# Optimization experiments

Measured on AMD Instinct MI355X. Metric: run time of the kernel, lower is better.

## Reference

```python
import jax, jax.numpy as jnp
import numpy as np

N_NODES = 50000


def gcn_conv(x, src, dst, W, b, n):
    # PyG GCNConv: h = x @ W; add self-loops; sym-norm aggregate; + bias
    h = x @ W
    loop = jnp.arange(n, dtype=src.dtype)
    s = jnp.concatenate([src, loop])
    d = jnp.concatenate([dst, loop])
    deg = jax.ops.segment_sum(jnp.ones(s.shape[0], h.dtype), d, num_segments=n)
    dinv = jnp.where(deg > 0, jax.lax.rsqrt(deg), 0.0)
    norm = dinv[s] * dinv[d]  # [E+n]
    msg = h[s] * norm[:, None]  # [E+n, C] gather
    out = jax.ops.segment_sum(msg, d, num_segments=n)  # scatter-add
    return out + b


def mlp_decode(z, src, dst, Wa, ba, Wb, bb):
    feat = jnp.concatenate([z[src], z[dst]], axis=1)  # [P, 2*out]
    hid = jax.nn.relu(feat @ Wa + ba)
    return hid @ Wb + bb  # [P, 1]


def setup_inputs() -> dict:
    key = jax.random.key(0)
    ks = jax.random.split(key, 12)
    in_c, hid_c, out_c = 128, 128, 64
    E, P = 800000, 200000
    x = jax.random.normal(ks[0], (N_NODES, in_c), dtype=jnp.float32)
    edge_index = jax.random.randint(ks[1], (2, E), 0, N_NODES, dtype=jnp.int64)
    pos_edge_index = jax.random.randint(ks[2], (2, P), 0, N_NODES, dtype=jnp.int64)
    neg_edge_index = jax.random.randint(ks[3], (2, P), 0, N_NODES, dtype=jnp.int64)
    s1 = 1.0 / np.sqrt(in_c)
    s2 = 1.0 / np.sqrt(hid_c)
    s3 = 1.0 / np.sqrt(2 * out_c)
    W1 = jax.random.uniform(ks[4], (in_c, hid_c), jnp.float32, -s1, s1)
    b1 = jnp.zeros((hid_c,), jnp.float32)
    W2 = jax.random.uniform(ks[5], (hid_c, out_c), jnp.float32, -s2, s2)
    b2 = jnp.zeros((out_c,), jnp.float32)
    Wa = jax.random.uniform(ks[6], (2 * out_c, hid_c), jnp.float32, -s3, s3)
    ba = jax.random.uniform(ks[7], (hid_c,), jnp.float32, -s3, s3)
    Wb = jax.random.uniform(ks[8], (hid_c, 1), jnp.float32, -s2, s2)
    bb = jax.random.uniform(ks[9], (1,), jnp.float32, -s2, s2)
    return {"x": x, "edge_index": edge_index, "pos_edge_index": pos_edge_index,
            "neg_edge_index": neg_edge_index, "W1": W1, "b1": b1, "W2": W2,
            "b2": b2, "Wa": Wa, "ba": ba, "Wb": Wb, "bb": bb}


def reference(x, edge_index, pos_edge_index, neg_edge_index,
              W1, b1, W2, b2, Wa, ba, Wb, bb):
    src, dst = edge_index[0], edge_index[1]
    n = x.shape[0]
    z = gcn_conv(x, src, dst, W1, b1, n)
    z = jax.nn.relu(z)  # dropout disabled in eval mode
    z = gcn_conv(z, src, dst, W2, b2, n)
    pos_pred = mlp_decode(z, pos_edge_index[0], pos_edge_index[1], Wa, ba, Wb, bb)
    neg_pred = mlp_decode(z, neg_edge_index[0], neg_edge_index[1], Wa, ba, Wb, bb)
    return (pos_pred, neg_pred)
```

## Files before the change

kernel.cpp:

```cpp
#include <hip/hip_runtime.h>
#include <hip/hip_bf16.h>

#define NODES 50000
#define NEDGE 800000
#define NPRED 200000

typedef __attribute__((ext_vector_type(8))) short bf16x8;
typedef __attribute__((ext_vector_type(8))) unsigned short u16x8;
typedef __attribute__((ext_vector_type(4))) float f32x4;

__device__ inline float bf2f(unsigned short u) {
    union { unsigned int i; float f; } v; v.i = ((unsigned int)u) << 16; return v.f;
}
__device__ inline unsigned short f2bf(float f) {
    __hip_bfloat16 b = __float2bfloat16(f);
    return *(unsigned short*)&b;
}

__global__ __launch_bounds__(256) void deg_init(int* __restrict__ deg, int* __restrict__ fillc, int n) {
    int i = blockIdx.x * 256 + threadIdx.x;
    if (i < n) { deg[i] = 1; fillc[i] = 0; }
}

__global__ __launch_bounds__(256) void deg_count(const int* __restrict__ dstv, int* __restrict__ deg, int E) {
    int e = blockIdx.x * 256 + threadIdx.x;
    if (e < E) atomicAdd(&deg[dstv[e]], 1);
}

__global__ __launch_bounds__(256) void scan_bsum(const int* __restrict__ deg, int* __restrict__ bsum, int n) {
    __shared__ int s[256];
    int t = threadIdx.x, b = blockIdx.x;
    int base = b * 1024 + t * 4;
    int sum = 0;
#pragma unroll
    for (int j = 0; j < 4; ++j) { int i = base + j; if (i < n) sum += deg[i] - 1; }
    s[t] = sum; __syncthreads();
    for (int off = 128; off >= 1; off >>= 1) {
        if (t < off) s[t] += s[t + off];
        __syncthreads();
    }
    if (t == 0) bsum[b] = s[0];
}

__global__ void scan_boff(const int* __restrict__ bsum, int* __restrict__ boff, int nb,
                          int* __restrict__ row_ptr, int n) {
    int t = threadIdx.x;
    int v = (t < nb) ? bsum[t] : 0;
    int orig = v;
    for (int off = 1; off < 64; off <<= 1) {
        int u = __shfl_up(v, off, 64);
        if (t >= off) v += u;
    }
    boff[t] = v - orig;
    if (t == 63) row_ptr[n] = v;
}

__global__ __launch_bounds__(256) void scan_write(const int* __restrict__ deg, const int* __restrict__ boff,
                                                  int* __restrict__ row_ptr, float* __restrict__ dinv, int n) {
    __shared__ int s[256];
    int t = threadIdx.x, b = blockIdx.x;
    int base = b * 1024 + t * 4;
    int v[4]; int sum = 0;
#pragma unroll
    for (int j = 0; j < 4; ++j) { int i = base + j; v[j] = (i < n) ? (deg[i] - 1) : 0; sum += v[j]; }
    s[t] = sum; __syncthreads();
    for (int off = 1; off < 256; off <<= 1) {
        int u = (t >= off) ? s[t - off] : 0;
        __syncthreads();
        s[t] += u;
        __syncthreads();
    }
    int run = s[t] - sum + boff[b];
#pragma unroll
    for (int j = 0; j < 4; ++j) {
        int i = base + j;
        if (i < n) { row_ptr[i] = run; run += v[j]; dinv[i] = rsqrtf((float)deg[i]); }
    }
}

__global__ __launch_bounds__(256) void csr_fill(const int* __restrict__ ei, const int* __restrict__ row_ptr,
                                                int* __restrict__ fillc, int* __restrict__ colv, int E) {
    int e = blockIdx.x * 256 + threadIdx.x;
    if (e < E) {
        int s = ei[e];
        int d = ei[E + e];
        int p = row_ptr[d] + atomicAdd(&fillc[d], 1);
        colv[p] = s;
    }
}

__global__ __launch_bounds__(256) void perm_all(const float* __restrict__ W1, const float* __restrict__ W2,
                                                const float* __restrict__ Wa,
                                                unsigned short* __restrict__ pW1,
                                                unsigned short* __restrict__ pW2,
                                                unsigned short* __restrict__ pWa) {
    int t = blockIdx.x * 256 + threadIdx.x;
    if (t >= 5120) return;
    const float* W; unsigned short* P; int N;
    if (t < 2048)      { W = W1; P = pW1; N = 128; }
    else if (t < 3072) { W = W2; P = pW2; N = 64;  t -= 2048; }
    else               { W = Wa; P = pWa; N = 128; t -= 3072; }
    int lane = t & 63;
    int kt = (t >> 6) & 3;
    int nt = t >> 8;
    int n = nt * 16 + (lane & 15);
    int k0 = kt * 32 + (lane >> 4) * 8;
#pragma unroll
    for (int j = 0; j < 8; ++j) P[t * 8 + j] = f2bf(W[(k0 + j) * N + n]);
}

template <int NT, bool AFP32>
__global__ __launch_bounds__(256) void gemm_mfma(const void* __restrict__ Xv,
                                                 const unsigned short* __restrict__ perm,
                                                 unsigned short* __restrict__ H, int M) {
    int w = blockIdx.x * 4 + (threadIdx.x >> 6);
    int m0 = w * 16;
    if (m0 >= M) return;
    int lane = threadIdx.x & 63;
    int m = lane & 15, q = lane >> 4;
    size_t row = (size_t)(m0 + m);
    bf16x8 a[4];
    if (AFP32) {
        const float* X = (const float*)Xv;
#pragma unroll
        for (int kt = 0; kt < 4; ++kt) {
            float4 f0 = *(const float4*)&X[row * 128 + kt * 32 + q * 8];
            float4 f1 = *(const float4*)&X[row * 128 + kt * 32 + q * 8 + 4];
            bf16x8 av;
            av[0] = (short)f2bf(f0.x); av[1] = (short)f2bf(f0.y);
            av[2] = (short)f2bf(f0.z); av[3] = (short)f2bf(f0.w);
            av[4] = (short)f2bf(f1.x); av[5] = (short)f2bf(f1.y);
            av[6] = (short)f2bf(f1.z); av[7] = (short)f2bf(f1.w);
            a[kt] = av;
        }
    } else {
        const unsigned short* X = (const unsigned short*)Xv;
#pragma unroll
        for (int kt = 0; kt < 4; ++kt)
            a[kt] = *(const bf16x8*)&X[row * 128 + kt * 32 + q * 8];
    }
    const int N = NT * 16;
#pragma unroll
    for (int nt = 0; nt < NT; ++nt) {
        f32x4 c = {0.f, 0.f, 0.f, 0.f};
#pragma unroll
        for (int kt = 0; kt < 4; ++kt) {
            bf16x8 b = *(const bf16x8*)(perm + (size_t)((nt * 4 + kt) * 64 + lane) * 8);
            c = __builtin_amdgcn_mfma_f32_16x16x32_bf16(a[kt], b, c, 0, 0, 0);
        }
#pragma unroll
        for (int r = 0; r < 4; ++r)
            H[(size_t)(m0 + q * 4 + r) * N + nt * 16 + m] = f2bf(c[r]);
    }
}

template <int C, bool RELU>
__global__ __launch_bounds__(256) void agg_bf16(const unsigned short* __restrict__ h,
                                                const int* __restrict__ row_ptr, const int* __restrict__ colv,
                                                const float* __restrict__ dinv, const float* __restrict__ bias,
                                                unsigned short* __restrict__ out) {
    constexpr int TPN = C / 8;
    constexpr int NPB = 256 / TPN;
    int d = blockIdx.x * NPB + threadIdx.x / TPN;
    if (d >= NODES) return;
    int c8 = (threadIdx.x % TPN) * 8;
    float dv = dinv[d];
    float acc[8];
    u16x8 self = *(const u16x8*)&h[(size_t)d * C + c8];
#pragma unroll
    for (int j = 0; j < 8; ++j) acc[j] = bf2f(self[j]) * dv;
    int i = row_ptr[d], end = row_ptr[d + 1];
    for (; i + 3 < end; i += 4) {
        int s0 = colv[i], s1 = colv[i + 1], s2 = colv[i + 2], s3 = colv[i + 3];
        float w0 = dinv[s0], w1 = dinv[s1], w2 = dinv[s2], w3 = dinv[s3];
        u16x8 r0 = *(const u16x8*)&h[(size_t)s0 * C + c8];
        u16x8 r1 = *(const u16x8*)&h[(size_t)s1 * C + c8];
        u16x8 r2 = *(const u16x8*)&h[(size_t)s2 * C + c8];
        u16x8 r3 = *(const u16x8*)&h[(size_t)s3 * C + c8];
#pragma unroll
        for (int j = 0; j < 8; ++j)
            acc[j] += bf2f(r0[j]) * w0 + bf2f(r1[j]) * w1 + bf2f(r2[j]) * w2 + bf2f(r3[j]) * w3;
    }
    for (; i < end; ++i) {
        int s0 = colv[i];
        float w0 = dinv[s0];
        u16x8 r0 = *(const u16x8*)&h[(size_t)s0 * C + c8];
#pragma unroll
        for (int j = 0; j < 8; ++j) acc[j] += bf2f(r0[j]) * w0;
    }
    u16x8 ov;
#pragma unroll
    for (int j = 0; j < 8; ++j) {
        float o = acc[j] * dv + bias[c8 + j];
        if (RELU) o = fmaxf(o, 0.f);
        ov[j] = f2bf(o);
    }
    *(u16x8*)&out[(size_t)d * C + c8] = ov;
}

__global__ __launch_bounds__(256) void decode_mfma(const unsigned short* __restrict__ zb,
                                                   const int* __restrict__ pos, const int* __restrict__ neg,
                                                   const unsigned short* __restrict__ perm,
                                                   const float* __restrict__ ba, const float* __restrict__ Wb,
                                                   const float* __restrict__ bb, float* __restrict__ out, int P) {
    int lane = threadIdx.x & 63;
    int w = blockIdx.x * 4 + (threadIdx.x >> 6);
    int half = (w >= 6250);
    const int* src = half ? neg : pos;
    float* o = out + (half ? P : 0);
    int e0 = (half ? (w - 6250) : w) * 32;
    int m = lane & 15, q = lane >> 4;
    int eA = e0 + m, eB = e0 + 16 + m;
    int sA = src[eA], dA = src[P + eA];
    int sB = src[eB], dB = src[P + eB];
    bf16x8 a0[4], a1[4];
    a0[0] = *(const bf16x8*)(zb + (size_t)sA * 64 + q * 8);
    a0[1] = *(const bf16x8*)(zb + (size_t)sA * 64 + 32 + q * 8);
    a0[2] = *(const bf16x8*)(zb + (size_t)dA * 64 + q * 8);
    a0[3] = *(const bf16x8*)(zb + (size_t)dA * 64 + 32 + q * 8);
    a1[0] = *(const bf16x8*)(zb + (size_t)sB * 64 + q * 8);
    a1[1] = *(const bf16x8*)(zb + (size_t)sB * 64 + 32 + q * 8);
    a1[2] = *(const bf16x8*)(zb + (size_t)dB * 64 + q * 8);
    a1[3] = *(const bf16x8*)(zb + (size_t)dB * 64 + 32 + q * 8);
    float p0[4] = {0.f, 0.f, 0.f, 0.f};
    float p1[4] = {0.f, 0.f, 0.f, 0.f};
#pragma unroll
    for (int nt = 0; nt < 8; ++nt) {
        f32x4 c0 = {0.f, 0.f, 0.f, 0.f};
        f32x4 c1 = {0.f, 0.f, 0.f, 0.f};
#pragma unroll
        for (int kt = 0; kt < 4; ++kt) {
            bf16x8 b = *(const bf16x8*)(perm + (size_t)((nt * 4 + kt) * 64 + lane) * 8);
            c0 = __builtin_amdgcn_mfma_f32_16x16x32_bf16(a0[kt], b, c0, 0, 0, 0);
            c1 = __builtin_amdgcn_mfma_f32_16x16x32_bf16(a1[kt], b, c1, 0, 0, 0);
        }
        int ch = nt * 16 + m;
        float bav = ba[ch], wbv = Wb[ch];
#pragma unroll
        for (int r = 0; r < 4; ++r) {
            p0[r] += fmaxf(c0[r] + bav, 0.f) * wbv;
            p1[r] += fmaxf(c1[r] + bav, 0.f) * wbv;
        }
    }
#pragma unroll
    for (int off = 8; off >= 1; off >>= 1) {
#pragma unroll
        for (int r = 0; r < 4; ++r) {
            p0[r] += __shfl_xor(p0[r], off, 64);
            p1[r] += __shfl_xor(p1[r], off, 64);
        }
    }
    if (m == 0) {
        float bbv = bb[0];
#pragma unroll
        for (int r = 0; r < 4; ++r) {
            o[e0 + q * 4 + r] = p0[r] + bbv;
            o[e0 + 16 + q * 4 + r] = p1[r] + bbv;
        }
    }
}

extern "C" void kernel_launch(void* const* d_in, const int* in_sizes, int n_in,
                              void* d_out, int out_size, void* d_ws, size_t ws_size,
                              hipStream_t stream) {
    const int N = NODES, E = NEDGE, P = NPRED;
    const float* x  = (const float*)d_in[0];
    const int*   ei = (const int*)d_in[1];
    const int*  pos = (const int*)d_in[2];
    const int*  neg = (const int*)d_in[3];
    const float* W1 = (const float*)d_in[4];
    const float* b1 = (const float*)d_in[5];
    const float* W2 = (const float*)d_in[6];
    const float* b2 = (const float*)d_in[7];
    const float* Wa = (const float*)d_in[8];
    const float* ba = (const float*)d_in[9];
    const float* Wb = (const float*)d_in[10];
    const float* bb = (const float*)d_in[11];
    float* out = (float*)d_out;

    char* w = (char*)d_ws;
    auto alloc = [&](size_t bytes) { char* p = w; w += (bytes + 255) & ~(size_t)255; return p; };
    int*   deg     = (int*)alloc((size_t)N * 4);
    int*   fillc   = (int*)alloc((size_t)N * 4);
    int*   row_ptr = (int*)alloc((size_t)(N + 1) * 4);
    int*   colv    = (int*)alloc((size_t)E * 4);
    float* dinv    = (float*)alloc((size_t)N * 4);
    int*   bsum    = (int*)alloc(64 * 4);
    int*   boff    = (int*)alloc(64 * 4);
    unsigned short* h1b = (unsigned short*)alloc((size_t)N * 128 * 2);
    unsigned short* z1b = (unsigned short*)alloc((size_t)N * 128 * 2);
    unsigned short* h2b = (unsigned short*)alloc((size_t)N * 64 * 2);
    unsigned short* zb  = (unsigned short*)alloc((size_t)N * 64 * 2);
    unsigned short* pW1 = (unsigned short*)alloc(2048 * 8 * 2);
    unsigned short* pW2 = (unsigned short*)alloc(1024 * 8 * 2);
    unsigned short* pWa = (unsigned short*)alloc(2048 * 8 * 2);

    const int nb = (N + 1023) / 1024;
    deg_init<<<(N + 255) / 256, 256, 0, stream>>>(deg, fillc, N);
    deg_count<<<(E + 255) / 256, 256, 0, stream>>>(ei + E, deg, E);
    scan_bsum<<<nb, 256, 0, stream>>>(deg, bsum, N);
    scan_boff<<<1, 64, 0, stream>>>(bsum, boff, nb, row_ptr, N);
    scan_write<<<nb, 256, 0, stream>>>(deg, boff, row_ptr, dinv, N);
    csr_fill<<<(E + 255) / 256, 256, 0, stream>>>(ei, row_ptr, fillc, colv, E);

    perm_all<<<20, 256, 0, stream>>>(W1, W2, Wa, pW1, pW2, pWa);

    gemm_mfma<8, true><<<782, 256, 0, stream>>>(x, pW1, h1b, N);
    agg_bf16<128, true><<<N / 16, 256, 0, stream>>>(h1b, row_ptr, colv, dinv, b1, z1b);

    gemm_mfma<4, false><<<782, 256, 0, stream>>>(z1b, pW2, h2b, N);
    agg_bf16<64, false><<<(N + 31) / 32, 256, 0, stream>>>(h2b, row_ptr, colv, dinv, b2, zb);

    decode_mfma<<<3125, 256, 0, stream>>>(zb, pos, neg, pWa, ba, Wb, bb, out, P);
}
```

Before: 285.8 us.

## Precompute per-node decoder projections and decode edges by gathering U and V

The edge MLP's first layer is split algebraically: concat(z[s],z[d])@Wa becomes z[s]@Wa_top + z[d]@Wa_bot. Both halves are computed once per node (50k rows) in fp16 instead of per edge (400k edges). Each edge then gathers two 128-wide fp16 rows and does only bias, relu and a dot with Wb. The CSR build is also simplified: the fill counters start at row_ptr, and degrees are counted with vectorized int4 loads. This removes redundant MFMA work at the cost of extra per-node memory traffic, larger per-edge gathers, and fp16 rounding of the intermediate.

After: 289.1 us. About the same (+1.2%).

```diff
diff --git a/kernel.cpp b/kernel.cpp
--- a/kernel.cpp
+++ b/kernel.cpp
@@ -1,5 +1,6 @@
 #include <hip/hip_runtime.h>
 #include <hip/hip_bf16.h>
+#include <hip/hip_fp16.h>
 
 #define NODES 50000
 #define NEDGE 800000
@@ -16,15 +17,27 @@
     __hip_bfloat16 b = __float2bfloat16(f);
     return *(unsigned short*)&b;
 }
-
-__global__ __launch_bounds__(256) void deg_init(int* __restrict__ deg, int* __restrict__ fillc, int n) {
+__device__ inline float h2f(unsigned short u) {
+    __half h = *(__half*)&u; return __half2float(h);
+}
+__device__ inline unsigned short f2h(float f) {
+    __half h = __float2half(f); return *(unsigned short*)&h;
+}
+
+__global__ __launch_bounds__(256) void deg_init(int* __restrict__ deg, int n) {
     int i = blockIdx.x * 256 + threadIdx.x;
-    if (i < n) { deg[i] = 1; fillc[i] = 0; }
-}
-
-__global__ __launch_bounds__(256) void deg_count(const int* __restrict__ dstv, int* __restrict__ deg, int E) {
-    int e = blockIdx.x * 256 + threadIdx.x;
-    if (e < E) atomicAdd(&deg[dstv[e]], 1);
+    if (i < n) deg[i] = 1;
+}
+
+__global__ __launch_bounds__(256) void deg_count4(const int* __restrict__ dstv, int* __restrict__ deg, int E4) {
+    int i = blockIdx.x * 256 + threadIdx.x;
+    if (i < E4) {
+        int4 d4 = ((const int4*)dstv)[i];
+        atomicAdd(&deg[d4.x], 1);
+        atomicAdd(&deg[d4.y], 1);
+        atomicAdd(&deg[d4.z], 1);
+        atomicAdd(&deg[d4.w], 1);
+    }
 }
 
 __global__ __launch_bounds__(256) void scan_bsum(const int* __restrict__ deg, int* __restrict__ bsum, int n) {
@@ -56,7 +69,8 @@
 }
 
 __global__ __launch_bounds__(256) void scan_write(const int* __restrict__ deg, const int* __restrict__ boff,
-                                                  int* __restrict__ row_ptr, float* __restrict__ dinv, int n) {
+                                                  int* __restrict__ row_ptr, int* __restrict__ fillc,
+                                                  float* __restrict__ dinv, int n) {
     __shared__ int s[256];
     int t = threadIdx.x, b = blockIdx.x;
     int base = b * 1024 + t * 4;
@@ -74,17 +88,20 @@
 #pragma unroll
     for (int j = 0; j < 4; ++j) {
         int i = base + j;
-        if (i < n) { row_ptr[i] = run; run += v[j]; dinv[i] = rsqrtf((float)deg[i]); }
-    }
-}
-
-__global__ __launch_bounds__(256) void csr_fill(const int* __restrict__ ei, const int* __restrict__ row_ptr,
+        if (i < n) {
+            row_ptr[i] = run; fillc[i] = run; run += v[j];
+            dinv[i] = rsqrtf((float)deg[i]);
+        }
+    }
+}
+
+__global__ __launch_bounds__(256) void csr_fill(const int* __restrict__ ei,
                                                 int* __restrict__ fillc, int* __restrict__ colv, int E) {
     int e = blockIdx.x * 256 + threadIdx.x;
     if (e < E) {
         int s = ei[e];
         int d = ei[E + e];
-        int p = row_ptr[d] + atomicAdd(&fillc[d], 1);
+        int p = atomicAdd(&fillc[d], 1);
         colv[p] = s;
     }
 }
@@ -96,17 +113,29 @@
                                                 unsigned short* __restrict__ pWa) {
     int t = blockIdx.x * 256 + threadIdx.x;
     if (t >= 5120) return;
-    const float* W; unsigned short* P; int N;
-    if (t < 2048)      { W = W1; P = pW1; N = 128; }
-    else if (t < 3072) { W = W2; P = pW2; N = 64;  t -= 2048; }
-    else               { W = Wa; P = pWa; N = 128; t -= 3072; }
-    int lane = t & 63;
-    int kt = (t >> 6) & 3;
-    int nt = t >> 8;
-    int n = nt * 16 + (lane & 15);
-    int k0 = kt * 32 + (lane >> 4) * 8;
-#pragma unroll
-    for (int j = 0; j < 8; ++j) P[t * 8 + j] = f2bf(W[(k0 + j) * N + n]);
+    if (t < 3072) {
+        const float* W; unsigned short* P; int N;
+        if (t < 2048) { W = W1; P = pW1; N = 128; }
+        else          { W = W2; P = pW2; N = 64; t -= 2048; }
+        int lane = t & 63;
+        int kt = (t >> 6) & 3;
+        int nt = t >> 8;
+        int n = nt * 16 + (lane & 15);
+        int k0 = kt * 32 + (lane >> 4) * 8;
+#pragma unroll
+        for (int j = 0; j < 8; ++j) P[t * 8 + j] = f2bf(W[(k0 + j) * N + n]);
+    } else {
+        int tt = t - 3072;
+        int h = tt >> 10;
+        int r = tt & 1023;
+        int lane = r & 63;
+        int kt = (r >> 6) & 1;
+        int nt = r >> 7;
+        int n = nt * 16 + (lane & 15);
+        int k0 = h * 64 + kt * 32 + (lane >> 4) * 8;
+#pragma unroll
+        for (int j = 0; j < 8; ++j) pWa[tt * 8 + j] = f2bf(Wa[(k0 + j) * 128 + n]);
+    }
 }
 
 template <int NT, bool AFP32>
@@ -198,66 +227,71 @@
     *(u16x8*)&out[(size_t)d * C + c8] = ov;
 }
 
-__global__ __launch_bounds__(256) void decode_mfma(const unsigned short* __restrict__ zb,
+__global__ __launch_bounds__(256) void uv_gemm(const unsigned short* __restrict__ zb,
+                                               const unsigned short* __restrict__ pWa,
+                                               unsigned short* __restrict__ U, unsigned short* __restrict__ V,
+                                               int M) {
+    int w = blockIdx.x * 4 + (threadIdx.x >> 6);
+    int m0 = w * 16;
+    if (m0 >= M) return;
+    int lane = threadIdx.x & 63;
+    int m = lane & 15, q = lane >> 4;
+    size_t row = (size_t)(m0 + m);
+    bf16x8 a0 = *(const bf16x8*)&zb[row * 64 + q * 8];
+    bf16x8 a1 = *(const bf16x8*)&zb[row * 64 + 32 + q * 8];
+#pragma unroll
+    for (int h = 0; h < 2; ++h) {
+        unsigned short* O = h ? V : U;
+        const unsigned short* p = pWa + (size_t)h * 1024 * 8;
+#pragma unroll
+        for (int nt = 0; nt < 8; ++nt) {
+            bf16x8 b0 = *(const bf16x8*)(p + (size_t)((nt * 2 + 0) * 64 + lane) * 8);
+            bf16x8 b1 = *(const bf16x8*)(p + (size_t)((nt * 2 + 1) * 64 + lane) * 8);
+            f32x4 c = {0.f, 0.f, 0.f, 0.f};
+            c = __builtin_amdgcn_mfma_f32_16x16x32_bf16(a0, b0, c, 0, 0, 0);
+            c = __builtin_amdgcn_mfma_f32_16x16x32_bf16(a1, b1, c, 0, 0, 0);
+#pragma unroll
+            for (int r = 0; r < 4; ++r)
+                O[(size_t)(m0 + q * 4 + r) * 128 + nt * 16 + m] = f2h(c[r]);
+        }
+    }
+}
+
+__global__ __launch_bounds__(256) void edge_decode(const unsigned short* __restrict__ U,
+                                                   const unsigned short* __restrict__ V,
                                                    const int* __restrict__ pos, const int* __restrict__ neg,
-                                                   const unsigned short* __restrict__ perm,
                                                    const float* __restrict__ ba, const float* __restrict__ Wb,
                                                    const float* __restrict__ bb, float* __restrict__ out, int P) {
-    int lane = threadIdx.x & 63;
-    int w = blockIdx.x * 4 + (threadIdx.x >> 6);
-    int half = (w >= 6250);
+    __shared__ float sba[128], sWb[128];
+    int tid = threadIdx.x;
+    if (tid < 128) sba[tid] = ba[tid];
+    else sWb[tid - 128] = Wb[tid - 128];
+    __syncthreads();
+    int half = (blockIdx.x >= 6250);
     const int* src = half ? neg : pos;
     float* o = out + (half ? P : 0);
-    int e0 = (half ? (w - 6250) : w) * 32;
-    int m = lane & 15, q = lane >> 4;
-    int eA = e0 + m, eB = e0 + 16 + m;
-    int sA = src[eA], dA = src[P + eA];
-    int sB = src[eB], dB = src[P + eB];
-    bf16x8 a0[4], a1[4];
-    a0[0] = *(const bf16x8*)(zb + (size_t)sA * 64 + q * 8);
-    a0[1] = *(const bf16x8*)(zb + (size_t)sA * 64 + 32 + q * 8);
-    a0[2] = *(const bf16x8*)(zb + (size_t)dA * 64 + q * 8);
-    a0[3] = *(const bf16x8*)(zb + (size_t)dA * 64 + 32 + q * 8);
-    a1[0] = *(const bf16x8*)(zb + (size_t)sB * 64 + q * 8);
-    a1[1] = *(const bf16x8*)(zb + (size_t)sB * 64 + 32 + q * 8);
-    a1[2] = *(const bf16x8*)(zb + (size_t)dB * 64 + q * 8);
-    a1[3] = *(const bf16x8*)(zb + (size_t)dB * 64 + 32 + q * 8);
-    float p0[4] = {0.f, 0.f, 0.f, 0.f};
-    float p1[4] = {0.f, 0.f, 0.f, 0.f};
-#pragma unroll
-    for (int nt = 0; nt < 8; ++nt) {
-        f32x4 c0 = {0.f, 0.f, 0.f, 0.f};
-        f32x4 c1 = {0.f, 0.f, 0.f, 0.f};
-#pragma unroll
-        for (int kt = 0; kt < 4; ++kt) {
-            bf16x8 b = *(const bf16x8*)(perm + (size_t)((nt * 4 + kt) * 64 + lane) * 8);
-            c0 = __builtin_amdgcn_mfma_f32_16x16x32_bf16(a0[kt], b, c0, 0, 0, 0);
-            c1 = __builtin_amdgcn_mfma_f32_16x16x32_bf16(a1[kt], b, c1, 0, 0, 0);
-        }
-        int ch = nt * 16 + m;
-        float bav = ba[ch], wbv = Wb[ch];
-#pragma unroll
-        for (int r = 0; r < 4; ++r) {
-            p0[r] += fmaxf(c0[r] + bav, 0.f) * wbv;
-            p1[r] += fmaxf(c1[r] + bav, 0.f) * wbv;
-        }
-    }
-#pragma unroll
-    for (int off = 8; off >= 1; off >>= 1) {
-#pragma unroll
-        for (int r = 0; r < 4; ++r) {
-            p0[r] += __shfl_xor(p0[r], off, 64);
-            p1[r] += __shfl_xor(p1[r], off, 64);
-        }
-    }
-    if (m == 0) {
-        float bbv = bb[0];
-#pragma unroll
-        for (int r = 0; r < 4; ++r) {
-            o[e0 + q * 4 + r] = p0[r] + bbv;
-            o[e0 + 16 + q * 4 + r] = p1[r] + bbv;
-        }
-    }
+    int b = half ? (int)blockIdx.x - 6250 : (int)blockIdx.x;
+    int lane = tid & 63;
+    int wv = tid >> 6;
+    int e = b * 32 + wv * 8 + (lane >> 3);
+    int ch0 = (lane & 7) * 16;
+    int s = src[e], d = src[P + e];
+    u16x8 u0 = *(const u16x8*)&U[(size_t)s * 128 + ch0];
+    u16x8 u1 = *(const u16x8*)&U[(size_t)s * 128 + ch0 + 8];
+    u16x8 v0 = *(const u16x8*)&V[(size_t)d * 128 + ch0];
+    u16x8 v1 = *(const u16x8*)&V[(size_t)d * 128 + ch0 + 8];
+    float acc = 0.f;
+#pragma unroll
+    for (int j = 0; j < 8; ++j) {
+        float a = h2f(u0[j]) + h2f(v0[j]) + sba[ch0 + j];
+        acc += fmaxf(a, 0.f) * sWb[ch0 + j];
+        float c = h2f(u1[j]) + h2f(v1[j]) + sba[ch0 + 8 + j];
+        acc += fmaxf(c, 0.f) * sWb[ch0 + 8 + j];
+    }
+    acc += __shfl_xor(acc, 1, 64);
+    acc += __shfl_xor(acc, 2, 64);
+    acc += __shfl_xor(acc, 4, 64);
+    if ((lane & 7) == 0) o[e] = acc + bb[0];
 }
 
 extern "C" void kernel_launch(void* const* d_in, const int* in_sizes, int n_in,
@@ -291,17 +325,19 @@
     unsigned short* z1b = (unsigned short*)alloc((size_t)N * 128 * 2);
     unsigned short* h2b = (unsigned short*)alloc((size_t)N * 64 * 2);
     unsigned short* zb  = (unsigned short*)alloc((size_t)N * 64 * 2);
+    unsigned short* Ut  = (unsigned short*)alloc((size_t)N * 128 * 2);
+    unsigned short* Vt  = (unsigned short*)alloc((size_t)N * 128 * 2);
     unsigned short* pW1 = (unsigned short*)alloc(2048 * 8 * 2);
     unsigned short* pW2 = (unsigned short*)alloc(1024 * 8 * 2);
     unsigned short* pWa = (unsigned short*)alloc(2048 * 8 * 2);
 
     const int nb = (N + 1023) / 1024;
-    deg_init<<<(N + 255) / 256, 256, 0, stream>>>(deg, fillc, N);
-    deg_count<<<(E + 255) / 256, 256, 0, stream>>>(ei + E, deg, E);
+    deg_init<<<(N + 255) / 256, 256, 0, stream>>>(deg, N);
+    deg_count4<<<(E / 4 + 255) / 256, 256, 0, stream>>>(ei + E, deg, E / 4);
     scan_bsum<<<nb, 256, 0, stream>>>(deg, bsum, N);
     scan_boff<<<1, 64, 0, stream>>>(bsum, boff, nb, row_ptr, N);
-    scan_write<<<nb, 256, 0, stream>>>(deg, boff, row_ptr, dinv, N);
-    csr_fill<<<(E + 255) / 256, 256, 0, stream>>>(ei, row_ptr, fillc, colv, E);
+    scan_write<<<nb, 256, 0, stream>>>(deg, boff, row_ptr, fillc, dinv, N);
+    csr_fill<<<(E + 255) / 256, 256, 0, stream>>>(ei, fillc, colv, E);
 
     perm_all<<<20, 256, 0, stream>>>(W1, W2, Wa, pW1, pW2, pWa);
 
@@ -311,5 +347,6 @@
     gemm_mfma<4, false><<<782, 256, 0, stream>>>(z1b, pW2, h2b, N);
     agg_bf16<64, false><<<(N + 31) / 32, 256, 0, stream>>>(h2b, row_ptr, colv, dinv, b2, zb);
 
-    decode_mfma<<<3125, 256, 0, stream>>>(zb, pos, neg, pWa, ba, Wb, bb, out, P);
-}
+    uv_gemm<<<782, 256, 0, stream>>>(zb, pWa, Ut, Vt, N);
+    edge_decode<<<12500, 256, 0, stream>>>(Ut, Vt, pos, neg, ba, Wb, bb, out, P);
+}
```

## Record edge ranks in count pass and software-pipeline the decode gathers

Applied to the files above, without the earlier changes.

The degree-count pass now records each edge's atomic rank, so the CSR fill becomes a plain scatter with no second round of atomics. Both edge passes use int4 vector loads, and a memset replaces the init kernel. The decode kernel makes each wave handle four 32-edge groups, prefetching indices two steps ahead and double-buffering the gathered z fragments so gather latency overlaps the MFMA work. It also hoists the bias and Wb loads and stores results as float4. The cost is an extra E-sized rank buffer and more register pressure in decode, which spreads the work over fewer waves.

New measurement: 260.6 us. -8.8%, faster.

```diff
diff --git a/kernel.cpp b/kernel.cpp
--- a/kernel.cpp
+++ b/kernel.cpp
@@ -1,5 +1,6 @@
 #include <hip/hip_runtime.h>
 #include <hip/hip_bf16.h>
+#include <hip/hip_fp16.h>
 
 #define NODES 50000
 #define NEDGE 800000
@@ -17,23 +18,27 @@
     return *(unsigned short*)&b;
 }
 
-__global__ __launch_bounds__(256) void deg_init(int* __restrict__ deg, int* __restrict__ fillc, int n) {
+__global__ __launch_bounds__(256) void rank_count4(const int* __restrict__ dstv, int* __restrict__ cnt,
+                                                   int* __restrict__ rank, int E4) {
     int i = blockIdx.x * 256 + threadIdx.x;
-    if (i < n) { deg[i] = 1; fillc[i] = 0; }
-}
-
-__global__ __launch_bounds__(256) void deg_count(const int* __restrict__ dstv, int* __restrict__ deg, int E) {
-    int e = blockIdx.x * 256 + threadIdx.x;
-    if (e < E) atomicAdd(&deg[dstv[e]], 1);
-}
-
-__global__ __launch_bounds__(256) void scan_bsum(const int* __restrict__ deg, int* __restrict__ bsum, int n) {
+    if (i < E4) {
+        int4 d4 = ((const int4*)dstv)[i];
+        int4 r4;
+        r4.x = atomicAdd(&cnt[d4.x], 1);
+        r4.y = atomicAdd(&cnt[d4.y], 1);
+        r4.z = atomicAdd(&cnt[d4.z], 1);
+        r4.w = atomicAdd(&cnt[d4.w], 1);
+        ((int4*)rank)[i] = r4;
+    }
+}
+
+__global__ __launch_bounds__(256) void scan_bsum(const int* __restrict__ cnt, int* __restrict__ bsum, int n) {
     __shared__ int s[256];
     int t = threadIdx.x, b = blockIdx.x;
     int base = b * 1024 + t * 4;
     int sum = 0;
 #pragma unroll
-    for (int j = 0; j < 4; ++j) { int i = base + j; if (i < n) sum += deg[i] - 1; }
+    for (int j = 0; j < 4; ++j) { int i = base + j; if (i < n) sum += cnt[i]; }
     s[t] = sum; __syncthreads();
     for (int off = 128; off >= 1; off >>= 1) {
         if (t < off) s[t] += s[t + off];
@@ -55,14 +60,14 @@
     if (t == 63) row_ptr[n] = v;
 }
 
-__global__ __launch_bounds__(256) void scan_write(const int* __restrict__ deg, const int* __restrict__ boff,
+__global__ __launch_bounds__(256) void scan_write(const int* __restrict__ cnt, const int* __restrict__ boff,
                                                   int* __restrict__ row_ptr, float* __restrict__ dinv, int n) {
     __shared__ int s[256];
     int t = threadIdx.x, b = blockIdx.x;
     int base = b * 1024 + t * 4;
     int v[4]; int sum = 0;
 #pragma unroll
-    for (int j = 0; j < 4; ++j) { int i = base + j; v[j] = (i < n) ? (deg[i] - 1) : 0; sum += v[j]; }
+    for (int j = 0; j < 4; ++j) { int i = base + j; v[j] = (i < n) ? cnt[i] : 0; sum += v[j]; }
     s[t] = sum; __syncthreads();
     for (int off = 1; off < 256; off <<= 1) {
         int u = (t >= off) ? s[t - off] : 0;
@@ -74,18 +79,24 @@
 #pragma unroll
     for (int j = 0; j < 4; ++j) {
         int i = base + j;
-        if (i < n) { row_ptr[i] = run; run += v[j]; dinv[i] = rsqrtf((float)deg[i]); }
-    }
-}
-
-__global__ __launch_bounds__(256) void csr_fill(const int* __restrict__ ei, const int* __restrict__ row_ptr,
-                                                int* __restrict__ fillc, int* __restrict__ colv, int E) {
-    int e = blockIdx.x * 256 + threadIdx.x;
-    if (e < E) {
-        int s = ei[e];
-        int d = ei[E + e];
-        int p = row_ptr[d] + atomicAdd(&fillc[d], 1);
-        colv[p] = s;
+        if (i < n) {
+            row_ptr[i] = run; run += v[j];
+            dinv[i] = rsqrtf((float)(v[j] + 1));
+        }
+    }
+}
+
+__global__ __launch_bounds__(256) void csr_fill2(const int* __restrict__ ei, const int* __restrict__ rank,
+                                                 const int* __restrict__ row_ptr, int* __restrict__ colv, int E4) {
+    int i = blockIdx.x * 256 + threadIdx.x;
+    if (i < E4) {
+        int4 s4 = ((const int4*)ei)[i];
+        int4 d4 = ((const int4*)(ei + NEDGE))[i];
+        int4 r4 = ((const int4*)rank)[i];
+        colv[row_ptr[d4.x] + r4.x] = s4.x;
+        colv[row_ptr[d4.y] + r4.y] = s4.y;
+        colv[row_ptr[d4.z] + r4.z] = s4.z;
+        colv[row_ptr[d4.w] + r4.w] = s4.w;
     }
 }
 
@@ -198,64 +209,87 @@
     *(u16x8*)&out[(size_t)d * C + c8] = ov;
 }
 
-__global__ __launch_bounds__(256) void decode_mfma(const unsigned short* __restrict__ zb,
-                                                   const int* __restrict__ pos, const int* __restrict__ neg,
-                                                   const unsigned short* __restrict__ perm,
-                                                   const float* __restrict__ ba, const float* __restrict__ Wb,
-                                                   const float* __restrict__ bb, float* __restrict__ out, int P) {
+__global__ __launch_bounds__(256) void decode_mfma2(const unsigned short* __restrict__ zb,
+                                                    const int* __restrict__ pos, const int* __restrict__ neg,
+                                                    const unsigned short* __restrict__ perm,
+                                                    const float* __restrict__ ba, const float* __restrict__ Wb,
+                                                    const float* __restrict__ bb, float* __restrict__ out, int P) {
     int lane = threadIdx.x & 63;
     int w = blockIdx.x * 4 + (threadIdx.x >> 6);
-    int half = (w >= 6250);
-    const int* src = half ? neg : pos;
-    float* o = out + (half ? P : 0);
-    int e0 = (half ? (w - 6250) : w) * 32;
+    int g0 = w * 4;
+    if (g0 >= 12500) return;
     int m = lane & 15, q = lane >> 4;
-    int eA = e0 + m, eB = e0 + 16 + m;
-    int sA = src[eA], dA = src[P + eA];
-    int sB = src[eB], dB = src[P + eB];
-    bf16x8 a0[4], a1[4];
-    a0[0] = *(const bf16x8*)(zb + (size_t)sA * 64 + q * 8);
-    a0[1] = *(const bf16x8*)(zb + (size_t)sA * 64 + 32 + q * 8);
-    a0[2] = *(const bf16x8*)(zb + (size_t)dA * 64 + q * 8);
-    a0[3] = *(const bf16x8*)(zb + (size_t)dA * 64 + 32 + q * 8);
-    a1[0] = *(const bf16x8*)(zb + (size_t)sB * 64 + q * 8);
-    a1[1] = *(const bf16x8*)(zb + (size_t)sB * 64 + 32 + q * 8);
-    a1[2] = *(const bf16x8*)(zb + (size_t)dB * 64 + q * 8);
-    a1[3] = *(const bf16x8*)(zb + (size_t)dB * 64 + 32 + q * 8);
-    float p0[4] = {0.f, 0.f, 0.f, 0.f};
-    float p1[4] = {0.f, 0.f, 0.f, 0.f};
-#pragma unroll
-    for (int nt = 0; nt < 8; ++nt) {
-        f32x4 c0 = {0.f, 0.f, 0.f, 0.f};
-        f32x4 c1 = {0.f, 0.f, 0.f, 0.f};
-#pragma unroll
-        for (int kt = 0; kt < 4; ++kt) {
-            bf16x8 b = *(const bf16x8*)(perm + (size_t)((nt * 4 + kt) * 64 + lane) * 8);
-            c0 = __builtin_amdgcn_mfma_f32_16x16x32_bf16(a0[kt], b, c0, 0, 0, 0);
-            c1 = __builtin_amdgcn_mfma_f32_16x16x32_bf16(a1[kt], b, c1, 0, 0, 0);
-        }
-        int ch = nt * 16 + m;
-        float bav = ba[ch], wbv = Wb[ch];
-#pragma unroll
-        for (int r = 0; r < 4; ++r) {
-            p0[r] += fmaxf(c0[r] + bav, 0.f) * wbv;
-            p1[r] += fmaxf(c1[r] + bav, 0.f) * wbv;
-        }
-    }
-#pragma unroll
-    for (int off = 8; off >= 1; off >>= 1) {
-#pragma unroll
-        for (int r = 0; r < 4; ++r) {
-            p0[r] += __shfl_xor(p0[r], off, 64);
-            p1[r] += __shfl_xor(p1[r], off, 64);
-        }
-    }
-    if (m == 0) {
-        float bbv = bb[0];
-#pragma unroll
-        for (int r = 0; r < 4; ++r) {
-            o[e0 + q * 4 + r] = p0[r] + bbv;
-            o[e0 + 16 + q * 4 + r] = p1[r] + bbv;
+    float bav[8], wbv[8];
+#pragma unroll
+    for (int nt = 0; nt < 8; ++nt) { bav[nt] = ba[nt * 16 + m]; wbv[nt] = Wb[nt * 16 + m]; }
+    float bbv = bb[0];
+
+    int idxS[3][2], idxD[3][2], base[3];
+    bf16x8 A[2][8];
+
+    auto loadIdx = [&](int it) {
+        int slot = it % 3;
+        int g = g0 + it;
+        int half = (g >= 6250) ? 1 : 0;
+        const int* src = half ? neg : pos;
+        int e0 = (g - half * 6250) * 32;
+        base[slot] = half * P + e0;
+        int eA = e0 + m, eB = e0 + 16 + m;
+        idxS[slot][0] = src[eA]; idxD[slot][0] = src[P + eA];
+        idxS[slot][1] = src[eB]; idxD[slot][1] = src[P + eB];
+    };
+    auto loadFrags = [&](int it) {
+        int slot = it % 3, buf = it & 1;
+        size_t s0 = (size_t)idxS[slot][0] * 64, d0 = (size_t)idxD[slot][0] * 64;
+        size_t s1 = (size_t)idxS[slot][1] * 64, d1 = (size_t)idxD[slot][1] * 64;
+        A[buf][0] = *(const bf16x8*)(zb + s0 + q * 8);
+        A[buf][1] = *(const bf16x8*)(zb + s0 + 32 + q * 8);
+        A[buf][2] = *(const bf16x8*)(zb + d0 + q * 8);
+        A[buf][3] = *(const bf16x8*)(zb + d0 + 32 + q * 8);
+        A[buf][4] = *(const bf16x8*)(zb + s1 + q * 8);
+        A[buf][5] = *(const bf16x8*)(zb + s1 + 32 + q * 8);
+        A[buf][6] = *(const bf16x8*)(zb + d1 + q * 8);
+        A[buf][7] = *(const bf16x8*)(zb + d1 + 32 + q * 8);
+    };
+
+    loadIdx(0); loadIdx(1); loadFrags(0);
+#pragma unroll
+    for (int it = 0; it < 4; ++it) {
+        if (it + 2 < 4) loadIdx(it + 2);
+        if (it + 1 < 4) loadFrags(it + 1);
+        int buf = it & 1;
+        float p0[4] = {0.f, 0.f, 0.f, 0.f};
+        float p1[4] = {0.f, 0.f, 0.f, 0.f};
+#pragma unroll
+        for (int nt = 0; nt < 8; ++nt) {
+            f32x4 c0 = {0.f, 0.f, 0.f, 0.f};
+            f32x4 c1 = {0.f, 0.f, 0.f, 0.f};
+#pragma unroll
+            for (int kt = 0; kt < 4; ++kt) {
+                bf16x8 b = *(const bf16x8*)(perm + (size_t)((nt * 4 + kt) * 64 + lane) * 8);
+                c0 = __builtin_amdgcn_mfma_f32_16x16x32_bf16(A[buf][kt], b, c0, 0, 0, 0);
+                c1 = __builtin_amdgcn_mfma_f32_16x16x32_bf16(A[buf][4 + kt], b, c1, 0, 0, 0);
+            }
+#pragma unroll
+            for (int r = 0; r < 4; ++r) {
+                p0[r] += fmaxf(c0[r] + bav[nt], 0.f) * wbv[nt];
+                p1[r] += fmaxf(c1[r] + bav[nt], 0.f) * wbv[nt];
+            }
+        }
+#pragma unroll
+        for (int off = 1; off <= 8; off <<= 1) {
+#pragma unroll
+            for (int r = 0; r < 4; ++r) {
+                p0[r] += __shfl_xor(p0[r], off, 64);
+                p1[r] += __shfl_xor(p1[r], off, 64);
+            }
+        }
+        if (m == 0) {
+            int slot = it % 3;
+            float4 st0 = { p0[0] + bbv, p0[1] + bbv, p0[2] + bbv, p0[3] + bbv };
+            float4 st1 = { p1[0] + bbv, p1[1] + bbv, p1[2] + bbv, p1[3] + bbv };
+            *(float4*)&out[base[slot] + q * 4] = st0;
+            *(float4*)&out[base[slot] + 16 + q * 4] = st1;
         }
     }
 }
@@ -280,8 +314,8 @@
 
     char* w = (char*)d_ws;
     auto alloc = [&](size_t bytes) { char* p = w; w += (bytes + 255) & ~(size_t)255; return p; };
-    int*   deg     = (int*)alloc((size_t)N * 4);
-    int*   fillc   = (int*)alloc((size_t)N * 4);
+    int*   cnt     = (int*)alloc((size_t)N * 4);
+    int*   rankb   = (int*)alloc((size_t)E * 4);
     int*   row_ptr = (int*)alloc((size_t)(N + 1) * 4);
     int*   colv    = (int*)alloc((size_t)E * 4);
     float* dinv    = (float*)alloc((size_t)N * 4);
@@ -296,12 +330,12 @@
     unsigned short* pWa = (unsigned short*)alloc(2048 * 8 * 2);
 
     const int nb = (N + 1023) / 1024;
-    deg_init<<<(N + 255) / 256, 256, 0, stream>>>(deg, fillc, N);
-    deg_count<<<(E + 255) / 256, 256, 0, stream>>>(ei + E, deg, E);
-    scan_bsum<<<nb, 256, 0, stream>>>(deg, bsum, N);
+    hipMemsetAsync(cnt, 0, (size_t)N * 4, stream);
+    rank_count4<<<(E / 4 + 255) / 256, 256, 0, stream>>>(ei + E, cnt, rankb, E / 4);
+    scan_bsum<<<nb, 256, 0, stream>>>(cnt, bsum, N);
     scan_boff<<<1, 64, 0, stream>>>(bsum, boff, nb, row_ptr, N);
-    scan_write<<<nb, 256, 0, stream>>>(deg, boff, row_ptr, dinv, N);
-    csr_fill<<<(E + 255) / 256, 256, 0, stream>>>(ei, row_ptr, fillc, colv, E);
+    scan_write<<<nb, 256, 0, stream>>>(cnt, boff, row_ptr, dinv, N);
+    csr_fill2<<<(E / 4 + 255) / 256, 256, 0, stream>>>(ei, rankb, row_ptr, colv, E / 4);
 
     perm_all<<<20, 256, 0, stream>>>(W1, W2, Wa, pW1, pW2, pWa);
 
@@ -311,5 +345,5 @@
     gemm_mfma<4, false><<<782, 256, 0, stream>>>(z1b, pW2, h2b, N);
     agg_bf16<64, false><<<(N + 31) / 32, 256, 0, stream>>>(h2b, row_ptr, colv, dinv, b2, zb);
 
-    decode_mfma<<<3125, 256, 0, stream>>>(zb, pos, neg, pWa, ba, Wb, bb, out, P);
-}
+    decode_mfma2<<<782, 256, 0, stream>>>(zb, pos, neg, pWa, ba, Wb, bb, out, P);
+}
```
